# Optimization experiments

Measured on AMD Instinct MI355X. Metric: run time of the kernel, lower is better.

The kernel has to match this reference:

```python
import math
import jax, jax.numpy as jnp
import numpy as np

NUM_HEADS = 16
HEAD_DIM = 128
CTX = 4096

def _rope_tables(head_dim, context_length, theta_base=10000.0):
    inv_freq = 1.0 / (theta_base ** (np.arange(0, head_dim, 2)[: head_dim // 2].astype(np.float32) / head_dim))
    pos = np.arange(context_length, dtype=np.float32)
    ang = pos[:, None] * inv_freq[None, :]
    ang = np.concatenate([ang, ang], axis=1)  # [ctx, head_dim]
    return jnp.asarray(np.cos(ang), jnp.float32), jnp.asarray(np.sin(ang), jnp.float32)

def _apply_rope(x, cos, sin):
    # x: [b, h, s, d]
    s, d = x.shape[2], x.shape[3]
    x1, x2 = x[..., : d // 2], x[..., d // 2 :]
    rotated = jnp.concatenate([-x2, x1], axis=-1)
    c = cos[:s][None, None]
    sn = sin[:s][None, None]
    return x * c + rotated * sn

def setup_inputs() -> dict:
    key = jax.random.key(0)
    kx, kq, kk, kv, ko = jax.random.split(key, 5)
    B, S, H = 2, 2048, 2048
    scale = 1.0 / math.sqrt(H)
    x = jax.random.normal(kx, (B, S, H), jnp.float32)
    Wq = jax.random.normal(kq, (H, H), jnp.float32) * scale
    Wk = jax.random.normal(kk, (H, H), jnp.float32) * scale
    Wv = jax.random.normal(kv, (H, H), jnp.float32) * scale
    Wo = jax.random.normal(ko, (H, H), jnp.float32) * scale
    cos, sin = _rope_tables(HEAD_DIM, CTX)
    return {"x": x, "Wq": Wq, "Wk": Wk, "Wv": Wv, "Wo": Wo, "cos": cos, "sin": sin}

def reference(x, Wq, Wk, Wv, Wo, cos, sin):
    B, S, Hd = x.shape
    nh, hd = NUM_HEADS, HEAD_DIM
    # nn.Linear(no bias): y = x @ W.T
    q = jnp.einsum('bsh,oh->bso', x, Wq).reshape(B, S, nh, hd).transpose(0, 2, 1, 3)
    k = jnp.einsum('bsh,oh->bso', x, Wk).reshape(B, S, nh, hd).transpose(0, 2, 1, 3)
    v = jnp.einsum('bsh,oh->bso', x, Wv).reshape(B, S, nh, hd).transpose(0, 2, 1, 3)
    q = _apply_rope(q, cos, sin)
    k = _apply_rope(k, cos, sin)
    # NOTE: faithful to source bug: scores are divided by (1/sqrt(d)),
    # i.e. MULTIPLIED by sqrt(head_dim).
    scores = jnp.einsum('bhqd,bhkd->bhqk', q, k) * math.sqrt(hd)
    causal = jnp.triu(jnp.ones((S, S), bool), k=1)
    scores = jnp.where(causal[None, None], -jnp.inf, scores)
    attn = jax.nn.softmax(scores, axis=-1)
    ctx = jnp.einsum('bhqk,bhkd->bhqd', attn, v)
    ctx = ctx.transpose(0, 2, 1, 3).reshape(B, S, Hd)
    return jnp.einsum('bsh,oh->bso', ctx, Wo)
```

## Files before the change

### kernel.cpp

```cpp
#include <hip/hip_runtime.h>

typedef unsigned short u16;
typedef __attribute__((ext_vector_type(8))) _Float16 f16x8;
typedef __attribute__((ext_vector_type(4))) float f32x4;

#define S_CTX 2048
#define DMODEL 2048

#define WAITVM(N) asm volatile("s_waitcnt vmcnt(" #N ")" ::: "memory")
#define SBAR() __builtin_amdgcn_s_barrier()

__device__ __forceinline__ u16 f2h(float f) {
  _Float16 h = (_Float16)f; u16 u; __builtin_memcpy(&u, &h, 2); return u;
}
__device__ __forceinline__ float h2f(u16 u) {
  _Float16 h; __builtin_memcpy(&h, &u, 2); return (float)h;
}
__device__ __forceinline__ void gload16(const u16* g, u16* l) {
  __builtin_amdgcn_global_load_lds(
      (const __attribute__((address_space(1))) unsigned int*)g,
      (__attribute__((address_space(3))) unsigned int*)l, 16, 0, 0);
}

__global__ void split_all(const float* __restrict__ x, const float* __restrict__ Wq,
                          const float* __restrict__ Wk, const float* __restrict__ Wv,
                          const float* __restrict__ Wo,
                          u16* xh, u16* xl, u16* Wqh, u16* Wql,
                          u16* Wkh, u16* Wkl, u16* Wvh, u16* Woh) {
  size_t i = (size_t)blockIdx.x * 256 + threadIdx.x;
  const size_t NX = 8388608, NW = 4194304;
  if (i < NX) {
    float v = x[i];
    u16 h = f2h(v);
    xh[i] = h; xl[i] = f2h(v - h2f(h));
  } else {
    size_t j = i - NX;
    int wsel = (int)(j >> 22);
    size_t o = j & (NW - 1);
    if (wsel == 0) { float v = Wq[o] * 64.f; u16 h = f2h(v); Wqh[o] = h; Wql[o] = f2h(v - h2f(h)); }
    else if (wsel == 1) { float v = Wk[o] * 64.f; u16 h = f2h(v); Wkh[o] = h; Wkl[o] = f2h(v - h2f(h)); }
    else if (wsel == 2) { Wvh[o] = f2h(Wv[o] * 64.f); }
    else { Woh[o] = f2h(Wo[o] * 64.f); }
  }
}

__device__ __forceinline__ void xcd_map_gemm(int& m0, int& n0) {
  const int lin = blockIdx.x | (blockIdx.y << 4);
  const int k = lin & 7, j = lin >> 3;
  const int by = ((k >> 1) << 3) | (j >> 3);
  const int bx = ((k & 1) << 3) | (j & 7);
  m0 = by << 7; n0 = bx << 7;
}

template <int NT, int MODE>
__device__ __forceinline__ void gemm_core(
    u16* sm, const u16* __restrict__ Am, const u16* __restrict__ Alm,
    const u16* __restrict__ Bm, const u16* __restrict__ Blm,
    float* __restrict__ Cf, u16* __restrict__ Ch,
    const float* __restrict__ cosT, const float* __restrict__ sinT,
    int N, int K, int m0, int n0, float oscale) {
  const int tid = threadIdx.x;
  const int w = tid >> 6, lane = tid & 63;
  const int quad = lane >> 4, l16 = lane & 15;
  const int wm = (w >> 1) << 6, wn = (w & 1) << 6;
  const int lrow = lane >> 2, lcol = (lane & 3) << 3;
  const int lcs = lcol ^ (((lrow >> 1) & 3) << 3);
  const int qsw = (quad << 3) ^ (((l16 >> 1) & 3) << 3);

  auto stageH = [&](int bufb, int k0) {
#pragma unroll
    for (int j = 0; j < 2; ++j) {
      int r = w * 32 + j * 16 + lrow;
      int lb = bufb + (w * 32 + j * 16) * 32;
      size_t ga = (size_t)(m0 + r) * K + k0 + lcs;
      size_t gb = (size_t)(n0 + r) * K + k0 + lcs;
      gload16(Am + ga, &sm[lb]);
      gload16(Bm + gb, &sm[lb + 4096]);
    }
  };
  auto stageL = [&](int bufb, int k0) {
#pragma unroll
    for (int j = 0; j < 2; ++j) {
      int r = w * 32 + j * 16 + lrow;
      int lb = bufb + (w * 32 + j * 16) * 32;
      size_t ga = (size_t)(m0 + r) * K + k0 + lcs;
      size_t gb = (size_t)(n0 + r) * K + k0 + lcs;
      gload16(Blm + gb, &sm[lb + 8192]);
      gload16(Alm + ga, &sm[lb + 12288]);
    }
  };

  f32x4 acc[4][4];
#pragma unroll
  for (int i = 0; i < 4; ++i)
#pragma unroll
    for (int n = 0; n < 4; ++n) acc[i][n] = (f32x4){0.f, 0.f, 0.f, 0.f};

  const int NTL = K >> 5;

  if (NT == 3) {
    stageH(0, 0);
    stageL(0, 0);
    for (int t = 0; t < NTL; ++t) {
      const int cur = (t & 1) << 14;
      const int nxt = 16384 - cur;
      const int k0n = (t + 1) << 5;
      const bool more = (t + 1 < NTL);

      WAITVM(4);
      SBAR();
      f16x8 ah[4], bh[4];
#pragma unroll
      for (int i = 0; i < 4; ++i)
        ah[i] = *(const f16x8*)&sm[cur + (wm + i * 16 + l16) * 32 + qsw];
#pragma unroll
      for (int n = 0; n < 4; ++n)
        bh[n] = *(const f16x8*)&sm[cur + 4096 + (wn + n * 16 + l16) * 32 + qsw];
      if (more) { stageH(nxt, k0n); stageL(nxt, k0n); }
#pragma unroll
      for (int i = 0; i < 4; ++i)
#pragma unroll
        for (int n = 0; n < 4; ++n)
          acc[i][n] = __builtin_amdgcn_mfma_f32_16x16x32_f16(ah[i], bh[n], acc[i][n], 0, 0, 0);

      if (more) { WAITVM(8); } else { WAITVM(0); }
      SBAR();
      f16x8 bl[4], al[4];
#pragma unroll
      for (int n = 0; n < 4; ++n)
        bl[n] = *(const f16x8*)&sm[cur + 8192 + (wn + n * 16 + l16) * 32 + qsw];
#pragma unroll
      for (int i = 0; i < 4; ++i)
        al[i] = *(const f16x8*)&sm[cur + 12288 + (wm + i * 16 + l16) * 32 + qsw];
#pragma unroll
      for (int i = 0; i < 4; ++i)
#pragma unroll
        for (int n = 0; n < 4; ++n) {
          acc[i][n] = __builtin_amdgcn_mfma_f32_16x16x32_f16(ah[i], bl[n], acc[i][n], 0, 0, 0);
          acc[i][n] = __builtin_amdgcn_mfma_f32_16x16x32_f16(al[i], bh[n], acc[i][n], 0, 0, 0);
        }
    }
  } else {
    stageH(0, 0);
    stageH(8192, 32);
    for (int t = 0; t < NTL; ++t) {
      const int cur = (t % 3) * 8192;
      if (t + 1 < NTL) { WAITVM(4); } else { WAITVM(0); }
      SBAR();
      f16x8 ah[4], bh[4];
#pragma unroll
      for (int i = 0; i < 4; ++i)
        ah[i] = *(const f16x8*)&sm[cur + (wm + i * 16 + l16) * 32 + qsw];
#pragma unroll
      for (int n = 0; n < 4; ++n)
        bh[n] = *(const f16x8*)&sm[cur + 4096 + (wn + n * 16 + l16) * 32 + qsw];
      if (t + 2 < NTL) stageH(((t + 2) % 3) * 8192, (t + 2) << 5);
#pragma unroll
      for (int i = 0; i < 4; ++i)
#pragma unroll
        for (int n = 0; n < 4; ++n)
          acc[i][n] = __builtin_amdgcn_mfma_f32_16x16x32_f16(ah[i], bh[n], acc[i][n], 0, 0, 0);
    }
  }

  if (MODE == 3) {
    float* fs = (float*)sm;
    const int p = w >> 1;
#pragma unroll
    for (int i = 0; i < 4; ++i) {
      __syncthreads();
#pragma unroll
      for (int n = 0; n < 4; ++n)
#pragma unroll
        for (int r = 0; r < 4; ++r)
          fs[p * 2048 + (quad * 4 + r) * 128 + wn + n * 16 + l16] = acc[i][n][r];
      __syncthreads();
#pragma unroll
      for (int n = 0; n < 4; ++n) {
        const int col = wn + n * 16 + l16;
        const int cc = col ^ 64;
        const float sgn = (col < 64) ? -1.f : 1.f;
#pragma unroll
        for (int r = 0; r < 4; ++r) {
          const int row16 = quad * 4 + r;
          const int grow = m0 + wm + i * 16 + row16;
          const int s = grow & (S_CTX - 1);
          const float c = cosT[s * 128 + col];
          const float sn = sinT[s * 128 + col];
          const float x = fs[p * 2048 + row16 * 128 + col];
          const float xp = fs[p * 2048 + row16 * 128 + cc];
          Ch[(size_t)grow * N + n0 + col] = f2h((x * c + sgn * xp * sn) * oscale);
        }
      }
    }
    return;
  }
#pragma unroll
  for (int i = 0; i < 4; ++i)
#pragma unroll
    for (int n = 0; n < 4; ++n) {
      const int row0 = m0 + wm + i * 16 + quad * 4;
      const int col = n0 + wn + n * 16 + l16;
      if (MODE == 0) {
#pragma unroll
        for (int r = 0; r < 4; ++r) Cf[(size_t)(row0 + r) * N + col] = acc[i][n][r] * oscale;
      } else {
        int brow = row0 >> 11, s0 = row0 & 2047;
        int hh = col >> 7, d = col & 127;
        ushort4 pk;
        pk.x = f2h(acc[i][n][0]);
        pk.y = f2h(acc[i][n][1]);
        pk.z = f2h(acc[i][n][2]);
        pk.w = f2h(acc[i][n][3]);
        *(ushort4*)(Ch + ((size_t)(brow * 16 + hh) * 128 + d) * 2048 + s0) = pk;
      }
    }
}

__global__ __launch_bounds__(256) void qkv_kernel(
    const u16* __restrict__ xh, const u16* __restrict__ xl,
    const u16* __restrict__ Wqh, const u16* __restrict__ Wql,
    const u16* __restrict__ Wkh, const u16* __restrict__ Wkl,
    const u16* __restrict__ Wvh,
    const float* __restrict__ cosT, const float* __restrict__ sinT,
    u16* qh, u16* kh, u16* vt) {
  __shared__ u16 sm[32768];
  int m0, n0;
  xcd_map_gemm(m0, n0);
  const float qs = 0.002762135864009951f;
  if (blockIdx.z == 0)
    gemm_core<3, 3>(sm, xh, xl, Wqh, Wql, nullptr, qh, cosT, sinT, DMODEL, DMODEL, m0, n0, qs);
  else if (blockIdx.z == 1)
    gemm_core<3, 3>(sm, xh, xl, Wkh, Wkl, nullptr, kh, cosT, sinT, DMODEL, DMODEL, m0, n0, 1.f);
  else
    gemm_core<1, 2>(sm, xh, nullptr, Wvh, nullptr, nullptr, vt, nullptr, nullptr, DMODEL, DMODEL, m0, n0, 1.f);
}

__global__ __launch_bounds__(256) void out_kernel(
    const u16* __restrict__ ch, const u16* __restrict__ Woh, float* __restrict__ out) {
  __shared__ u16 sm[24576];
  int m0, n0;
  xcd_map_gemm(m0, n0);
  gemm_core<1, 0>(sm, ch, nullptr, Woh, nullptr, out, nullptr, nullptr, nullptr, DMODEL, DMODEL,
                  m0, n0, 1.f / 4096.f);
}

__global__ __launch_bounds__(512) void attn_kernel(
    const u16* __restrict__ Qh, const u16* __restrict__ Kh,
    const u16* __restrict__ VT, u16* __restrict__ Ch) {
  const int lin = blockIdx.x | (blockIdx.y << 3);
  const int xk = lin & 7, lj = lin >> 3;
  const int bh = (xk << 2) | (lj >> 3);
  const int bx = lj & 7;
  const int b = bh >> 4, h = bh & 15;
  const int tid = threadIdx.x;
  const int w = tid >> 6, lane = tid & 63;
  const int quad = lane >> 4, l16 = lane & 15;

  __shared__ u16 sKh[64 * 136];
  __shared__ u16 sVt[128 * 72];
  __shared__ u16 sPb[8 * 1088];
  u16* sP = &sPb[w * 1088];

  const size_t bhbase = (size_t)b * S_CTX * DMODEL + (size_t)h * 128;
  const size_t vtbase = (size_t)bh * 128 * 2048;

  int kr[2], kc[2], vr[2], vc[2];
#pragma unroll
  for (int j = 0; j < 2; ++j) {
    int c = j * 512 + tid;
    kr[j] = c >> 4; kc[j] = (c & 15) << 3;
    vr[j] = c >> 3; vc[j] = (c & 7) << 3;
  }

#pragma unroll 1
  for (int pass = 0; pass < 2; ++pass) {
    const int qt = pass ? bx : 15 - bx;

    const int qr0 = qt * 128 + w * 16;
    const size_t qoff = bhbase + (size_t)(qr0 + l16) * DMODEL;
    f16x8 qf[4];
#pragma unroll
    for (int c = 0; c < 4; ++c) qf[c] = *(const f16x8*)(Qh + qoff + c * 32 + quad * 8);

    f32x4 oacc[8];
#pragma unroll
    for (int d = 0; d < 8; ++d) oacc[d] = (f32x4){0.f, 0.f, 0.f, 0.f};
    float m_r[4] = {-INFINITY, -INFINITY, -INFINITY, -INFINITY};
    float l_r[4] = {0.f, 0.f, 0.f, 0.f};

    f16x8 rkh[2], rvt[2];
#pragma unroll
    for (int j = 0; j < 2; ++j) {
      rkh[j] = *(const f16x8*)(Kh + bhbase + (size_t)kr[j] * DMODEL + kc[j]);
      rvt[j] = *(const f16x8*)(VT + vtbase + (size_t)vr[j] * 2048 + vc[j]);
    }

    const int nkt = 2 * qt + 2;
    for (int kt = 0; kt < nkt; ++kt) {
      __syncthreads();
#pragma unroll
      for (int j = 0; j < 2; ++j) {
        *(f16x8*)&sKh[kr[j] * 136 + kc[j]] = rkh[j];
        *(f16x8*)&sVt[vr[j] * 72 + vc[j]] = rvt[j];
      }
      __syncthreads();
      if (kt + 1 < nkt) {
#pragma unroll
        for (int j = 0; j < 2; ++j) {
          size_t g = bhbase + (size_t)((kt + 1) * 64 + kr[j]) * DMODEL + kc[j];
          rkh[j] = *(const f16x8*)(Kh + g);
          rvt[j] = *(const f16x8*)(VT + vtbase + (size_t)vr[j] * 2048 + (kt + 1) * 64 + vc[j]);
        }
      }

      const bool active = (kt * 64) <= (qr0 + 15);
      if (active) {
        f32x4 sacc[4];
#pragma unroll
        for (int n = 0; n < 4; ++n) sacc[n] = (f32x4){0.f, 0.f, 0.f, 0.f};
#pragma unroll
        for (int n = 0; n < 4; ++n)
#pragma unroll
          for (int c = 0; c < 4; ++c) {
            f16x8 kf = *(const f16x8*)&sKh[(n * 16 + l16) * 136 + c * 32 + quad * 8];
            sacc[n] = __builtin_amdgcn_mfma_f32_16x16x32_f16(qf[c], kf, sacc[n], 0, 0, 0);
          }

        float pm[4][4];
        float rowmax[4] = {-INFINITY, -INFINITY, -INFINITY, -INFINITY};
#pragma unroll
        for (int n = 0; n < 4; ++n)
#pragma unroll
          for (int r = 0; r < 4; ++r) {
            float sc = sacc[n][r];
            int qi = qr0 + quad * 4 + r;
            int ki = kt * 64 + n * 16 + l16;
            if (ki > qi) sc = -INFINITY;
            pm[n][r] = sc;
            rowmax[r] = fmaxf(rowmax[r], sc);
          }
#pragma unroll
        for (int off = 1; off < 16; off <<= 1)
#pragma unroll
          for (int r = 0; r < 4; ++r)
            rowmax[r] = fmaxf(rowmax[r], __shfl_xor(rowmax[r], off, 64));

        float alphav[4];
#pragma unroll
        for (int r = 0; r < 4; ++r) {
          float mnew = fmaxf(m_r[r], rowmax[r]);
          alphav[r] = __expf(m_r[r] - mnew);
          m_r[r] = mnew;
          l_r[r] *= alphav[r];
        }
        float rowsum[4] = {0.f, 0.f, 0.f, 0.f};
#pragma unroll
        for (int n = 0; n < 4; ++n)
#pragma unroll
          for (int r = 0; r < 4; ++r) {
            float p = __expf(pm[n][r] - m_r[r]);
            pm[n][r] = p;
            rowsum[r] += p;
          }
#pragma unroll
        for (int off = 1; off < 16; off <<= 1)
#pragma unroll
          for (int r = 0; r < 4; ++r) rowsum[r] += __shfl_xor(rowsum[r], off, 64);
#pragma unroll
        for (int r = 0; r < 4; ++r) l_r[r] += rowsum[r];

#pragma unroll
        for (int d = 0; d < 8; ++d)
#pragma unroll
          for (int r = 0; r < 4; ++r) oacc[d][r] *= alphav[r];

#pragma unroll
        for (int n = 0; n < 4; ++n)
#pragma unroll
          for (int r = 0; r < 4; ++r)
            sP[(quad * 4 + r) * 68 + n * 16 + l16] = f2h(pm[n][r]);

#pragma unroll
        for (int c = 0; c < 2; ++c) {
          f16x8 pf = *(const f16x8*)&sP[l16 * 68 + c * 32 + quad * 8];
#pragma unroll
          for (int d = 0; d < 8; ++d) {
            f16x8 vf = *(const f16x8*)&sVt[(d * 16 + l16) * 72 + c * 32 + quad * 8];
            oacc[d] = __builtin_amdgcn_mfma_f32_16x16x32_f16(pf, vf, oacc[d], 0, 0, 0);
          }
        }
      }
    }

    float invl[4];
#pragma unroll
    for (int r = 0; r < 4; ++r) invl[r] = 1.f / l_r[r];
#pragma unroll
    for (int d = 0; d < 8; ++d)
#pragma unroll
      for (int r = 0; r < 4; ++r) {
        int row = qr0 + quad * 4 + r;
        Ch[bhbase + (size_t)row * DMODEL + d * 16 + l16] = f2h(oacc[d][r] * invl[r]);
      }
  }
}

extern "C" void kernel_launch(void* const* d_in, const int* in_sizes, int n_in,
                              void* d_out, int out_size, void* d_ws, size_t ws_size,
                              hipStream_t stream) {
  const float* x    = (const float*)d_in[0];
  const float* Wq   = (const float*)d_in[1];
  const float* Wk   = (const float*)d_in[2];
  const float* Wv   = (const float*)d_in[3];
  const float* Wo   = (const float*)d_in[4];
  const float* cosT = (const float*)d_in[5];
  const float* sinT = (const float*)d_in[6];
  float* out = (float*)d_out;

  const size_t NX = 8388608;
  const size_t NW = 4194304;
  u16* p = (u16*)d_ws;
  u16* xh  = p; p += NX;  u16* xl  = p; p += NX;
  u16* Wqh = p; p += NW;  u16* Wql = p; p += NW;
  u16* Wkh = p; p += NW;  u16* Wkl = p; p += NW;
  u16* Wvh = p; p += NW;  u16* Woh = p; p += NW;
  u16* qh  = p; p += NX;  u16* kh  = p; p += NX;
  u16* vt  = p; p += NX;
  u16* ch  = p; p += NX;

  split_all<<<98304, 256, 0, stream>>>(x, Wq, Wk, Wv, Wo,
                                       xh, xl, Wqh, Wql, Wkh, Wkl, Wvh, Woh);

  qkv_kernel<<<dim3(16, 32, 3), 256, 0, stream>>>(xh, xl, Wqh, Wql, Wkh, Wkl, Wvh,
                                                  cosT, sinT, qh, kh, vt);

  attn_kernel<<<dim3(8, 32), 512, 0, stream>>>(qh, kh, vt, ch);

  out_kernel<<<dim3(16, 32), 256, 0, stream>>>(ch, Woh, out);
}
```

Before: 563.8 us.

## Split hi/lo staging in QKV GEMM, remap blocks across XCDs, raise MFMA priority

In the three-term QKV GEMM, the next tile's low-part loads are now issued only after the current low-part fragments are read. The mid-loop wait is tightened to match, so the high-part loads of the next tile overlap the first MFMA pass. Address arithmetic is hoisted into precomputed 32-bit offsets. QKV blocks are remapped so Q, K and V tiles interleave across XCDs for better L2 sharing of x, and the attention MFMA sections are wrapped in s_setprio to favour matrix issue. The hoisted int offsets assume the offsets fit in 32 bits, and the reordered waits rely on exact vmcnt accounting.

```diff
diff --git a/kernel.cpp b/kernel.cpp
--- a/kernel.cpp
+++ b/kernel.cpp
@@ -52,6 +52,16 @@
   m0 = by << 7; n0 = bx << 7;
 }
 
+__device__ __forceinline__ void xcd_map_qkv(int& z, int& m0, int& n0) {
+  const int lin = blockIdx.x | (blockIdx.y << 4) | (blockIdx.z << 9);
+  const int k = lin & 7, j = lin >> 3;
+  z = j % 3;
+  const int jj = j / 3;
+  const int by = ((k >> 1) << 3) | (jj >> 3);
+  const int bx = ((k & 1) << 3) | (jj & 7);
+  m0 = by << 7; n0 = bx << 7;
+}
+
 template <int NT, int MODE>
 __device__ __forceinline__ void gemm_core(
     u16* sm, const u16* __restrict__ Am, const u16* __restrict__ Alm,
@@ -67,27 +77,29 @@
   const int lcs = lcol ^ (((lrow >> 1) & 3) << 3);
   const int qsw = (quad << 3) ^ (((l16 >> 1) & 3) << 3);
 
+  const int r0 = w * 32 + lrow;
+  const int offA0 = (m0 + r0) * K + lcs;
+  const int offA1 = offA0 + (K << 4);
+  const int offB0 = (n0 + r0) * K + lcs;
+  const int offB1 = offB0 + (K << 4);
+  const int ld0 = (w * 32) * 32;
+  const int ld1 = (w * 32 + 16) * 32;
+
   auto stageH = [&](int bufb, int k0) {
-#pragma unroll
-    for (int j = 0; j < 2; ++j) {
-      int r = w * 32 + j * 16 + lrow;
-      int lb = bufb + (w * 32 + j * 16) * 32;
-      size_t ga = (size_t)(m0 + r) * K + k0 + lcs;
-      size_t gb = (size_t)(n0 + r) * K + k0 + lcs;
-      gload16(Am + ga, &sm[lb]);
-      gload16(Bm + gb, &sm[lb + 4096]);
-    }
+    const u16* A_k = Am + k0;
+    const u16* B_k = Bm + k0;
+    gload16(A_k + offA0, &sm[bufb + ld0]);
+    gload16(A_k + offA1, &sm[bufb + ld1]);
+    gload16(B_k + offB0, &sm[bufb + 4096 + ld0]);
+    gload16(B_k + offB1, &sm[bufb + 4096 + ld1]);
   };
   auto stageL = [&](int bufb, int k0) {
-#pragma unroll
-    for (int j = 0; j < 2; ++j) {
-      int r = w * 32 + j * 16 + lrow;
-      int lb = bufb + (w * 32 + j * 16) * 32;
-      size_t ga = (size_t)(m0 + r) * K + k0 + lcs;
-      size_t gb = (size_t)(n0 + r) * K + k0 + lcs;
-      gload16(Blm + gb, &sm[lb + 8192]);
-      gload16(Alm + ga, &sm[lb + 12288]);
-    }
+    const u16* Bl_k = Blm + k0;
+    const u16* Al_k = Alm + k0;
+    gload16(Bl_k + offB0, &sm[bufb + 8192 + ld0]);
+    gload16(Bl_k + offB1, &sm[bufb + 8192 + ld1]);
+    gload16(Al_k + offA0, &sm[bufb + 12288 + ld0]);
+    gload16(Al_k + offA1, &sm[bufb + 12288 + ld1]);
   };
 
   f32x4 acc[4][4];
@@ -116,14 +128,14 @@
 #pragma unroll
       for (int n = 0; n < 4; ++n)
         bh[n] = *(const f16x8*)&sm[cur + 4096 + (wn + n * 16 + l16) * 32 + qsw];
-      if (more) { stageH(nxt, k0n); stageL(nxt, k0n); }
+      if (more) stageH(nxt, k0n);
 #pragma unroll
       for (int i = 0; i < 4; ++i)
 #pragma unroll
         for (int n = 0; n < 4; ++n)
           acc[i][n] = __builtin_amdgcn_mfma_f32_16x16x32_f16(ah[i], bh[n], acc[i][n], 0, 0, 0);
 
-      if (more) { WAITVM(8); } else { WAITVM(0); }
+      if (more) { WAITVM(4); } else { WAITVM(0); }
       SBAR();
       f16x8 bl[4], al[4];
 #pragma unroll
@@ -132,6 +144,7 @@
 #pragma unroll
       for (int i = 0; i < 4; ++i)
         al[i] = *(const f16x8*)&sm[cur + 12288 + (wm + i * 16 + l16) * 32 + qsw];
+      if (more) stageL(nxt, k0n);
 #pragma unroll
       for (int i = 0; i < 4; ++i)
 #pragma unroll
@@ -225,12 +238,12 @@
     const float* __restrict__ cosT, const float* __restrict__ sinT,
     u16* qh, u16* kh, u16* vt) {
   __shared__ u16 sm[32768];
-  int m0, n0;
-  xcd_map_gemm(m0, n0);
+  int z, m0, n0;
+  xcd_map_qkv(z, m0, n0);
   const float qs = 0.002762135864009951f;
-  if (blockIdx.z == 0)
+  if (z == 0)
     gemm_core<3, 3>(sm, xh, xl, Wqh, Wql, nullptr, qh, cosT, sinT, DMODEL, DMODEL, m0, n0, qs);
-  else if (blockIdx.z == 1)
+  else if (z == 1)
     gemm_core<3, 3>(sm, xh, xl, Wkh, Wkl, nullptr, kh, cosT, sinT, DMODEL, DMODEL, m0, n0, 1.f);
   else
     gemm_core<1, 2>(sm, xh, nullptr, Wvh, nullptr, nullptr, vt, nullptr, nullptr, DMODEL, DMODEL, m0, n0, 1.f);
@@ -319,6 +332,7 @@
         f32x4 sacc[4];
 #pragma unroll
         for (int n = 0; n < 4; ++n) sacc[n] = (f32x4){0.f, 0.f, 0.f, 0.f};
+        __builtin_amdgcn_s_setprio(1);
 #pragma unroll
         for (int n = 0; n < 4; ++n)
 #pragma unroll
@@ -326,6 +340,7 @@
             f16x8 kf = *(const f16x8*)&sKh[(n * 16 + l16) * 136 + c * 32 + quad * 8];
             sacc[n] = __builtin_amdgcn_mfma_f32_16x16x32_f16(qf[c], kf, sacc[n], 0, 0, 0);
           }
+        __builtin_amdgcn_s_setprio(0);
 
         float pm[4][4];
         float rowmax[4] = {-INFINITY, -INFINITY, -INFINITY, -INFINITY};
@@ -381,6 +396,7 @@
           for (int r = 0; r < 4; ++r)
             sP[(quad * 4 + r) * 68 + n * 16 + l16] = f2h(pm[n][r]);
 
+        __builtin_amdgcn_s_setprio(1);
 #pragma unroll
         for (int c = 0; c < 2; ++c) {
           f16x8 pf = *(const f16x8*)&sP[l16 * 68 + c * 32 + quad * 8];
@@ -390,6 +406,7 @@
             oacc[d] = __builtin_amdgcn_mfma_f32_16x16x32_f16(pf, vf, oacc[d], 0, 0, 0);
           }
         }
+        __builtin_amdgcn_s_setprio(0);
       }
     }
 
```

After: 597.2 us. 1.06x slower.
